# Kernel tuning notes

Hardware: AMD Instinct MI355X
Metric: run time of the kernel (lower is better)

## Reference

```python
import jax, jax.numpy as jnp
import numpy as np

B, N, L, U = 128, 32, 100, 1024  # batch, n agents, traj length, hidden units


def setup_inputs() -> dict:
    key = jax.random.key(0)
    ks = jax.random.split(key, 16)
    s = 0.02
    return {
        "x": jax.random.normal(ks[0], (B, 4 * N, L), dtype=jnp.float32),
        "edges": jax.random.uniform(ks[1], (B, N, N), dtype=jnp.float32),
        # traj MLP: 4*L -> U -> U -> 1  (weights stored as [in, out])
        "traj1_w": s * jax.random.normal(ks[2], (4 * L, U), dtype=jnp.float32),
        "traj1_b": jnp.zeros((U,), dtype=jnp.float32),
        "traj2_w": s * jax.random.normal(ks[3], (U, U), dtype=jnp.float32),
        "traj2_b": jnp.zeros((U,), dtype=jnp.float32),
        "traj3_w": s * jax.random.normal(ks[4], (U, 1), dtype=jnp.float32),
        "traj3_b": jnp.zeros((1,), dtype=jnp.float32),
        # interaction MLP: 8*L -> U -> U -> 1
        "int1_w": s * jax.random.normal(ks[5], (8 * L, U), dtype=jnp.float32),
        "int1_b": jnp.zeros((U,), dtype=jnp.float32),
        "int2_w": s * jax.random.normal(ks[6], (U, U), dtype=jnp.float32),
        "int2_b": jnp.zeros((U,), dtype=jnp.float32),
        "int3_w": s * jax.random.normal(ks[7], (U, 1), dtype=jnp.float32),
        "int3_b": jnp.zeros((1,), dtype=jnp.float32),
    }


def _mlp3(h, w1, b1, w2, b2, w3, b3):
    h = jax.nn.relu(h @ w1 + b1)
    h = jax.nn.relu(h @ w2 + b2)
    return h @ w3 + b3


def reference(x, edges, traj1_w, traj1_b, traj2_w, traj2_b, traj3_w, traj3_b,
              int1_w, int1_b, int2_w, int2_b, int3_w, int3_b):
    b = x.shape[0]
    n = edges.shape[1]
    length = x.shape[2]
    x4 = x.reshape(b, n, 4, length)  # [B, n, 4, L]

    # per-trajectory energy: (B*n, 4*L) -> MLP -> (B, n) -> sum over agents
    te = _mlp3(x4.reshape(b * n, 4 * length),
               traj1_w, traj1_b, traj2_w, traj2_b, traj3_w, traj3_b)
    traj_e = te.reshape(b, n).sum(axis=1, keepdims=True)  # [B, 1]

    # pairwise interaction energy: concat sender/receiver channels -> (B*n*n, 8*L)
    xi = jnp.broadcast_to(x4[:, :, None], (b, n, n, 4, length))  # row index c1
    xj = jnp.broadcast_to(x4[:, None, :], (b, n, n, 4, length))  # col index c2
    pair = jnp.concatenate([xi, xj], axis=3).reshape(b * n * n, 8 * length)
    ie = _mlp3(pair, int1_w, int1_b, int2_w, int2_b, int3_w, int3_b)
    int_e = (edges * ie.reshape(b, n, n)).sum(axis=(1, 2))[:, None]  # [B, 1]

    return traj_e + int_e  # [B, 1]
```

## Files before the change

kernel.cpp:

```cpp
#include <hip/hip_runtime.h>

typedef unsigned short u16;
typedef unsigned int u32;
typedef short bf16x8_t __attribute__((ext_vector_type(8)));
typedef float f32x4_t __attribute__((ext_vector_type(4)));

#define OFF_XB   (0)
#define SZ_XB    (4096*416*2)
#define OFF_WCAT (OFF_XB + SZ_XB)
#define SZ_WCAT  (3072*416*2)
#define OFF_W2T  (OFF_WCAT + SZ_WCAT)
#define SZ_W2    (1024*1024*2)
#define OFF_W2I  (OFF_W2T + SZ_W2)
#define OFF_T1   (OFF_W2I + SZ_W2)
#define SZ_T1    (4096*1024*2)
#define OFF_P    (OFF_T1 + SZ_T1)
#define SZ_PQ    (4096*1024*4)
#define OFF_Q    (OFF_P + SZ_PQ)

__device__ __forceinline__ u16 f2bf(float f) {
  union { float f; u32 u; } v; v.f = f;
  u32 r = v.u + 0x7fffu + ((v.u >> 16) & 1u);
  return (u16)(r >> 16);
}
__device__ __forceinline__ u32 pk2(float a, float b) {
  u32 ua = __float_as_uint(fmaxf(a, 0.f)) + 0x8000u;
  u32 ub = __float_as_uint(fmaxf(b, 0.f)) + 0x8000u;
  return __builtin_amdgcn_perm(ub, ua, 0x07060302);
}
__device__ __forceinline__ void gload_lds16(const void* g, void* l) {
  __builtin_amdgcn_global_load_lds(
      (const __attribute__((address_space(1))) void*)g,
      (__attribute__((address_space(3))) void*)l, 16, 0, 0);
}

__device__ __forceinline__ void stage_sw(const u16* g, int ld, int row0, int k0,
                                         u16* lds, int nrow64, int wave, int lane) {
  int c = ((lane & 3) - ((lane >> 2) & 3)) & 3;
  const u16* src0 = g + (size_t)(row0 + (lane >> 2)) * ld + k0 + c * 8;
#pragma unroll
  for (int it = 0; it < nrow64; ++it) {
    int rbase = it * 64 + wave * 16;
    gload_lds16(src0 + (size_t)rbase * ld, lds + rbase * 32);
  }
}
__device__ __forceinline__ bf16x8_t read_sw(const u16* lds, int row, int quad) {
  int s = (quad + row) & 3;
  return *(const bf16x8_t*)(lds + row * 32 + s * 8);
}

__global__ __launch_bounds__(256) void k_prep(
    const float* __restrict__ x, const float* __restrict__ t1w,
    const float* __restrict__ i1w, const float* __restrict__ t2w,
    const float* __restrict__ i2w, u16* __restrict__ Xb,
    u16* __restrict__ Wcat, u16* __restrict__ W2t, u16* __restrict__ W2i) {
  __shared__ float tb[32][33];
  int gy = blockIdx.y, tid = threadIdx.x;
  if (gy < 4096) {
    int k = blockIdx.x * 256 + tid;
    if (k < 416)
      Xb[(size_t)gy * 416 + k] = (k < 400) ? f2bf(x[(size_t)gy * 400 + k]) : (u16)0;
  } else if (gy < 7168) {
    int n = gy - 4096;
    int k = blockIdx.x * 256 + tid;
    if (k >= 416) return;
    float v = 0.f;
    if (k < 400) {
      if (n < 1024)      v = t1w[(size_t)k * 1024 + n];
      else if (n < 2048) v = i1w[(size_t)k * 1024 + (n - 1024)];
      else               v = i1w[(size_t)(400 + k) * 1024 + (n - 2048)];
    }
    Wcat[(size_t)n * 416 + k] = f2bf(v);
  } else {
    if (blockIdx.x) return;
    int t = gy - 7168;
    const float* W = (t < 1024) ? t2w : i2w;
    u16* Wt = (t < 1024) ? W2t : W2i;
    int tt = t & 1023;
    int n0 = (tt & 31) * 32, k0 = (tt >> 5) * 32;
    int tx = tid & 31, ty = tid >> 5;
#pragma unroll
    for (int i = 0; i < 32; i += 8)
      tb[ty + i][tx] = W[(size_t)(k0 + ty + i) * 1024 + n0 + tx];
    __syncthreads();
#pragma unroll
    for (int i = 0; i < 32; i += 8)
      Wt[(size_t)(n0 + ty + i) * 1024 + k0 + tx] = f2bf(tb[tx][ty + i]);
  }
}

__global__ __launch_bounds__(256) void k_gemm_l1(
    const u16* __restrict__ Xb, const u16* __restrict__ Wt,
    const float* __restrict__ b_t1, const float* __restrict__ b_i1,
    u16* __restrict__ T1, float* __restrict__ Pp, float* __restrict__ Qq) {
  __shared__ __align__(16) u16 al[128 * 32];
  __shared__ __align__(16) u16 bl[128 * 32];
  int tid = threadIdx.x, lane = tid & 63, wave = tid >> 6;
  int wr = wave & 1, wc = wave >> 1, ln = lane & 15, quad = lane >> 4;
  int m0 = blockIdx.x * 128, n0 = blockIdx.y * 128;
  f32x4_t acc[4][4];
#pragma unroll
  for (int i = 0; i < 4; ++i)
#pragma unroll
    for (int j = 0; j < 4; ++j) acc[i][j] = (f32x4_t){0.f, 0.f, 0.f, 0.f};

  for (int k0 = 0; k0 < 416; k0 += 32) {
    stage_sw(Xb, 416, m0, k0, al, 2, wave, lane);
    stage_sw(Wt, 416, n0, k0, bl, 2, wave, lane);
    __syncthreads();
    bf16x8_t af[4], bfr[4];
#pragma unroll
    for (int mt = 0; mt < 4; ++mt)
      af[mt] = read_sw(al, wr * 64 + mt * 16 + ln, quad);
#pragma unroll
    for (int nt = 0; nt < 4; ++nt)
      bfr[nt] = read_sw(bl, wc * 64 + nt * 16 + ln, quad);
#pragma unroll
    for (int mt = 0; mt < 4; ++mt)
#pragma unroll
      for (int nt = 0; nt < 4; ++nt)
        acc[mt][nt] = __builtin_amdgcn_mfma_f32_16x16x32_bf16(af[mt], bfr[nt], acc[mt][nt], 0, 0, 0);
    __syncthreads();
  }
  int seg = n0 >> 10;
#pragma unroll
  for (int nt = 0; nt < 4; ++nt) {
    int n_g = n0 + wc * 64 + nt * 16 + ln;
    int ns = n_g & 1023;
    float bias = (seg == 0) ? b_t1[ns] : (seg == 1 ? b_i1[ns] : 0.f);
#pragma unroll
    for (int mt = 0; mt < 4; ++mt) {
      f32x4_t c = acc[mt][nt];
#pragma unroll
      for (int r = 0; r < 4; ++r) {
        int m_g = m0 + wr * 64 + mt * 16 + quad * 4 + r;
        size_t idx = (size_t)m_g * 1024 + ns;
        float v = c[r] + bias;
        if (seg == 0)      T1[idx] = (u16)((__float_as_uint(fmaxf(v, 0.f)) + 0x8000u) >> 16);
        else if (seg == 1) Pp[idx] = v;
        else               Qq[idx] = v;
      }
    }
  }
}

__global__ __launch_bounds__(256) void k_traj23(
    const u16* __restrict__ T1, const u16* __restrict__ W2t,
    const float* __restrict__ b2, const float* __restrict__ w3,
    const float* __restrict__ b3, float* __restrict__ out) {
  __shared__ __align__(16) u16 al[128 * 32];
  __shared__ __align__(16) u16 bl[128 * 32];
  __shared__ float rowsum[128];
  int tid = threadIdx.x, lane = tid & 63, wave = tid >> 6;
  int wr = wave & 1, wc = wave >> 1, ln = lane & 15, quad = lane >> 4;
  int m0 = blockIdx.x * 128, n0 = blockIdx.y * 128;
  f32x4_t acc[4][4];
#pragma unroll
  for (int i = 0; i < 4; ++i)
#pragma unroll
    for (int j = 0; j < 4; ++j) acc[i][j] = (f32x4_t){0.f, 0.f, 0.f, 0.f};

  for (int k0 = 0; k0 < 1024; k0 += 32) {
    stage_sw(T1, 1024, m0, k0, al, 2, wave, lane);
    stage_sw(W2t, 1024, n0, k0, bl, 2, wave, lane);
    __syncthreads();
    bf16x8_t af[4], bfr[4];
#pragma unroll
    for (int mt = 0; mt < 4; ++mt)
      af[mt] = read_sw(al, wr * 64 + mt * 16 + ln, quad);
#pragma unroll
    for (int nt = 0; nt < 4; ++nt)
      bfr[nt] = read_sw(bl, wc * 64 + nt * 16 + ln, quad);
#pragma unroll
    for (int mt = 0; mt < 4; ++mt)
#pragma unroll
      for (int nt = 0; nt < 4; ++nt)
        acc[mt][nt] = __builtin_amdgcn_mfma_f32_16x16x32_bf16(af[mt], bfr[nt], acc[mt][nt], 0, 0, 0);
    __syncthreads();
  }
  float b2v[4], w3v[4];
#pragma unroll
  for (int nt = 0; nt < 4; ++nt) {
    int n = n0 + wc * 64 + nt * 16 + ln;
    b2v[nt] = b2[n]; w3v[nt] = w3[n];
  }
  if (tid < 128) rowsum[tid] = 0.f;
  __syncthreads();
#pragma unroll
  for (int mt = 0; mt < 4; ++mt) {
    float s[4] = {0.f, 0.f, 0.f, 0.f};
#pragma unroll
    for (int nt = 0; nt < 4; ++nt) {
      f32x4_t c = acc[mt][nt];
#pragma unroll
      for (int r = 0; r < 4; ++r) s[r] += fmaxf(c[r] + b2v[nt], 0.f) * w3v[nt];
    }
#pragma unroll
    for (int r = 0; r < 4; ++r) {
      for (int off = 1; off < 16; off <<= 1) s[r] += __shfl_xor(s[r], off);
      if (ln == 0) atomicAdd(&rowsum[wr * 64 + mt * 16 + quad * 4 + r], s[r]);
    }
  }
  __syncthreads();
  float contrib = 0.f;
  if (tid < 128) contrib = rowsum[tid] + (n0 == 0 ? b3[0] : 0.f);
  for (int off = 1; off < 32; off <<= 1) contrib += __shfl_xor(contrib, off);
  if ((lane & 31) == 0 && tid < 128) atomicAdd(&out[(m0 + tid) >> 5], contrib);
}

#define LDA_H 40
__device__ __forceinline__ void pack_h1(u16* dst, int rloc, int kh,
                                        float4 p0, float4 p1, float4 q0, float4 q1) {
  uint4 w;
  w.x = pk2(p0.x + q0.x, p0.y + q0.y);
  w.y = pk2(p0.z + q0.z, p0.w + q0.w);
  w.z = pk2(p1.x + q1.x, p1.y + q1.y);
  w.w = pk2(p1.z + q1.z, p1.w + q1.w);
  *(uint4*)(dst + rloc * LDA_H + kh) = w;
}

__global__ __launch_bounds__(256) void k_int_fused(
    const float* __restrict__ Pp, const float* __restrict__ Qq,
    const u16* __restrict__ W2t, const float* __restrict__ b2,
    const float* __restrict__ w3, const float* __restrict__ b3,
    const float* __restrict__ edges, float* __restrict__ out) {
  __shared__ __align__(16) u16 h1[2 * 64 * LDA_H];
  __shared__ __align__(16) u16 bl[2 * 256 * 32];
  __shared__ float rowsum[64];
  int tid = threadIdx.x, lane = tid & 63, wave = tid >> 6;
  int ln = lane & 15, quad = lane >> 4;
  int mtile = blockIdx.y;
  int n0 = blockIdx.x * 256;
  int b = mtile >> 4;
  int i0 = (mtile & 15) * 2;

  int rloc = tid >> 2;
  int kh = (tid & 3) * 8;
  const float* prow = Pp + ((size_t)(b * 32 + i0 + (rloc >> 5)) << 10) + kh;
  const float* qrow = Qq + ((size_t)(b * 32 + (rloc & 31)) << 10) + kh;

  f32x4_t acc[4][4];
#pragma unroll
  for (int i = 0; i < 4; ++i)
#pragma unroll
    for (int j = 0; j < 4; ++j) acc[i][j] = (f32x4_t){0.f, 0.f, 0.f, 0.f};

  float4 pA0, pA1, qA0, qA1;
  float4 pB0, pB1, qB0, qB1;

  {
    float4 t0 = *(const float4*)(prow),     t1 = *(const float4*)(prow + 4);
    float4 u0 = *(const float4*)(qrow),     u1 = *(const float4*)(qrow + 4);
    pack_h1(h1, rloc, kh, t0, t1, u0, u1);
    stage_sw(W2t, 1024, n0, 0, bl, 4, wave, lane);
    pA0 = *(const float4*)(prow + 32); pA1 = *(const float4*)(prow + 36);
    qA0 = *(const float4*)(qrow + 32); qA1 = *(const float4*)(qrow + 36);
  }
  __syncthreads();

  for (int kp = 0; kp < 1024; kp += 64) {
    {
      bf16x8_t af[4], bfr[4];
#pragma unroll
      for (int mt = 0; mt < 4; ++mt)
        af[mt] = *(const bf16x8_t*)(h1 + (mt * 16 + ln) * LDA_H + quad * 8);
#pragma unroll
      for (int nt = 0; nt < 4; ++nt)
        bfr[nt] = read_sw(bl, wave * 64 + nt * 16 + ln, quad);
      if (kp + 64 < 1024) {
        pB0 = *(const float4*)(prow + kp + 64); pB1 = *(const float4*)(prow + kp + 68);
        qB0 = *(const float4*)(qrow + kp + 64); qB1 = *(const float4*)(qrow + kp + 68);
      }
      stage_sw(W2t, 1024, n0, kp + 32, bl + 256 * 32, 4, wave, lane);
#pragma unroll
      for (int mt = 0; mt < 4; ++mt)
#pragma unroll
        for (int nt = 0; nt < 4; ++nt)
          acc[mt][nt] = __builtin_amdgcn_mfma_f32_16x16x32_bf16(af[mt], bfr[nt], acc[mt][nt], 0, 0, 0);
      pack_h1(h1 + 64 * LDA_H, rloc, kh, pA0, pA1, qA0, qA1);
      __syncthreads();
    }
    {
      bf16x8_t af[4], bfr[4];
#pragma unroll
      for (int mt = 0; mt < 4; ++mt)
        af[mt] = *(const bf16x8_t*)(h1 + 64 * LDA_H + (mt * 16 + ln) * LDA_H + quad * 8);
#pragma unroll
      for (int nt = 0; nt < 4; ++nt)
        bfr[nt] = read_sw(bl + 256 * 32, wave * 64 + nt * 16 + ln, quad);
      if (kp + 96 < 1024) {
        pA0 = *(const float4*)(prow + kp + 96); pA1 = *(const float4*)(prow + kp + 100);
        qA0 = *(const float4*)(qrow + kp + 96); qA1 = *(const float4*)(qrow + kp + 100);
      }
      if (kp + 64 < 1024)
        stage_sw(W2t, 1024, n0, kp + 64, bl, 4, wave, lane);
#pragma unroll
      for (int mt = 0; mt < 4; ++mt)
#pragma unroll
        for (int nt = 0; nt < 4; ++nt)
          acc[mt][nt] = __builtin_amdgcn_mfma_f32_16x16x32_bf16(af[mt], bfr[nt], acc[mt][nt], 0, 0, 0);
      if (kp + 64 < 1024)
        pack_h1(h1, rloc, kh, pB0, pB1, qB0, qB1);
      __syncthreads();
    }
  }

  float b2v[4], w3v[4];
#pragma unroll
  for (int nt = 0; nt < 4; ++nt) {
    int n = n0 + wave * 64 + nt * 16 + ln;
    b2v[nt] = b2[n]; w3v[nt] = w3[n];
  }
  if (tid < 64) rowsum[tid] = 0.f;
  __syncthreads();
#pragma unroll
  for (int mt = 0; mt < 4; ++mt) {
    float s[4] = {0.f, 0.f, 0.f, 0.f};
#pragma unroll
    for (int nt = 0; nt < 4; ++nt) {
      f32x4_t c = acc[mt][nt];
#pragma unroll
      for (int r = 0; r < 4; ++r) s[r] += fmaxf(c[r] + b2v[nt], 0.f) * w3v[nt];
    }
#pragma unroll
    for (int r = 0; r < 4; ++r) {
      for (int off = 1; off < 16; off <<= 1) s[r] += __shfl_xor(s[r], off);
      if (ln == 0) atomicAdd(&rowsum[mt * 16 + quad * 4 + r], s[r]);
    }
  }
  __syncthreads();
  if (wave == 0) {
    float ie = rowsum[lane] + (n0 == 0 ? b3[0] : 0.f);
    int i = i0 + (lane >> 5), j = lane & 31;
    float contrib = edges[(size_t)b * 1024 + i * 32 + j] * ie;
    for (int off = 1; off < 64; off <<= 1) contrib += __shfl_xor(contrib, off);
    if (lane == 0) atomicAdd(&out[b], contrib);
  }
}

extern "C" void kernel_launch(void* const* d_in, const int* in_sizes, int n_in,
                              void* d_out, int out_size, void* d_ws, size_t ws_size,
                              hipStream_t stream) {
  const float* x   = (const float*)d_in[0];
  const float* edges = (const float*)d_in[1];
  const float* t1w = (const float*)d_in[2];
  const float* t1b = (const float*)d_in[3];
  const float* t2w = (const float*)d_in[4];
  const float* t2b = (const float*)d_in[5];
  const float* t3w = (const float*)d_in[6];
  const float* t3b = (const float*)d_in[7];
  const float* i1w = (const float*)d_in[8];
  const float* i1b = (const float*)d_in[9];
  const float* i2w = (const float*)d_in[10];
  const float* i2b = (const float*)d_in[11];
  const float* i3w = (const float*)d_in[12];
  const float* i3b = (const float*)d_in[13];
  char* ws = (char*)d_ws;
  u16*   Xb   = (u16*)(ws + OFF_XB);
  u16*   Wcat = (u16*)(ws + OFF_WCAT);
  u16*   W2t  = (u16*)(ws + OFF_W2T);
  u16*   W2i  = (u16*)(ws + OFF_W2I);
  u16*   T1   = (u16*)(ws + OFF_T1);
  float* Pp   = (float*)(ws + OFF_P);
  float* Qq   = (float*)(ws + OFF_Q);
  float* out  = (float*)d_out;

  hipMemsetAsync(out, 0, 128 * sizeof(float), stream);
  k_prep<<<dim3(2, 9216), 256, 0, stream>>>(x, t1w, i1w, t2w, i2w, Xb, Wcat, W2t, W2i);
  k_gemm_l1<<<dim3(32, 24), 256, 0, stream>>>(Xb, Wcat, t1b, i1b, T1, Pp, Qq);
  k_traj23<<<dim3(32, 8), 256, 0, stream>>>(T1, W2t, t2b, t3w, t3b, out);
  k_int_fused<<<dim3(4, 2048), 256, 0, stream>>>(Pp, Qq, W2i, i2b, i3w, i3b, edges, out);
}
```

Baseline: 583.3 us.

## Load interaction W2 fragments directly from global in k-blocked layout, drop LDS staging

```diff
diff --git a/kernel.cpp b/kernel.cpp
--- a/kernel.cpp
+++ b/kernel.cpp
@@ -53,7 +53,7 @@
     const float* __restrict__ x, const float* __restrict__ t1w,
     const float* __restrict__ i1w, const float* __restrict__ t2w,
     const float* __restrict__ i2w, u16* __restrict__ Xb,
-    u16* __restrict__ Wcat, u16* __restrict__ W2t, u16* __restrict__ W2i) {
+    u16* __restrict__ Wcat, u16* __restrict__ W2t, u16* __restrict__ W2k) {
   __shared__ float tb[32][33];
   int gy = blockIdx.y, tid = threadIdx.x;
   if (gy < 4096) {
@@ -74,18 +74,23 @@
   } else {
     if (blockIdx.x) return;
     int t = gy - 7168;
-    const float* W = (t < 1024) ? t2w : i2w;
-    u16* Wt = (t < 1024) ? W2t : W2i;
     int tt = t & 1023;
     int n0 = (tt & 31) * 32, k0 = (tt >> 5) * 32;
     int tx = tid & 31, ty = tid >> 5;
+    const float* W = (t < 1024) ? t2w : i2w;
 #pragma unroll
     for (int i = 0; i < 32; i += 8)
       tb[ty + i][tx] = W[(size_t)(k0 + ty + i) * 1024 + n0 + tx];
     __syncthreads();
-#pragma unroll
-    for (int i = 0; i < 32; i += 8)
-      Wt[(size_t)(n0 + ty + i) * 1024 + k0 + tx] = f2bf(tb[tx][ty + i]);
+    if (t < 1024) {
+#pragma unroll
+      for (int i = 0; i < 32; i += 8)
+        W2t[(size_t)(n0 + ty + i) * 1024 + k0 + tx] = f2bf(tb[tx][ty + i]);
+    } else {
+#pragma unroll
+      for (int i = 0; i < 32; i += 8)
+        W2k[(size_t)(k0 >> 5) * 32768 + (size_t)(n0 + ty + i) * 32 + tx] = f2bf(tb[tx][ty + i]);
+    }
   }
 }
 
@@ -221,11 +226,10 @@
 
 __global__ __launch_bounds__(256) void k_int_fused(
     const float* __restrict__ Pp, const float* __restrict__ Qq,
-    const u16* __restrict__ W2t, const float* __restrict__ b2,
+    const u16* __restrict__ W2k, const float* __restrict__ b2,
     const float* __restrict__ w3, const float* __restrict__ b3,
     const float* __restrict__ edges, float* __restrict__ out) {
   __shared__ __align__(16) u16 h1[2 * 64 * LDA_H];
-  __shared__ __align__(16) u16 bl[2 * 256 * 32];
   __shared__ float rowsum[64];
   int tid = threadIdx.x, lane = tid & 63, wave = tid >> 6;
   int ln = lane & 15, quad = lane >> 4;
@@ -238,6 +242,7 @@
   int kh = (tid & 3) * 8;
   const float* prow = Pp + ((size_t)(b * 32 + i0 + (rloc >> 5)) << 10) + kh;
   const float* qrow = Qq + ((size_t)(b * 32 + (rloc & 31)) << 10) + kh;
+  const u16* bptr = W2k + (size_t)(n0 + wave * 64 + ln) * 32 + quad * 8;
 
   f32x4_t acc[4][4];
 #pragma unroll
@@ -245,62 +250,64 @@
 #pragma unroll
     for (int j = 0; j < 4; ++j) acc[i][j] = (f32x4_t){0.f, 0.f, 0.f, 0.f};
 
-  float4 pA0, pA1, qA0, qA1;
-  float4 pB0, pB1, qB0, qB1;
-
+  bf16x8_t bA[4], bB[4];
   {
     float4 t0 = *(const float4*)(prow),     t1 = *(const float4*)(prow + 4);
     float4 u0 = *(const float4*)(qrow),     u1 = *(const float4*)(qrow + 4);
     pack_h1(h1, rloc, kh, t0, t1, u0, u1);
-    stage_sw(W2t, 1024, n0, 0, bl, 4, wave, lane);
-    pA0 = *(const float4*)(prow + 32); pA1 = *(const float4*)(prow + 36);
-    qA0 = *(const float4*)(qrow + 32); qA1 = *(const float4*)(qrow + 36);
-  }
-  __syncthreads();
-
+#pragma unroll
+    for (int nt = 0; nt < 4; ++nt)
+      bA[nt] = *(const bf16x8_t*)(bptr + nt * 512);
+  }
+  __syncthreads();
+
+  float4 pN0, pN1, qN0, qN1;
   for (int kp = 0; kp < 1024; kp += 64) {
     {
-      bf16x8_t af[4], bfr[4];
+      int k0 = kp;
+      bf16x8_t af[4];
 #pragma unroll
       for (int mt = 0; mt < 4; ++mt)
         af[mt] = *(const bf16x8_t*)(h1 + (mt * 16 + ln) * LDA_H + quad * 8);
-#pragma unroll
-      for (int nt = 0; nt < 4; ++nt)
-        bfr[nt] = read_sw(bl, wave * 64 + nt * 16 + ln, quad);
-      if (kp + 64 < 1024) {
-        pB0 = *(const float4*)(prow + kp + 64); pB1 = *(const float4*)(prow + kp + 68);
-        qB0 = *(const float4*)(qrow + kp + 64); qB1 = *(const float4*)(qrow + kp + 68);
+      if (k0 + 32 < 1024) {
+        pN0 = *(const float4*)(prow + k0 + 32); pN1 = *(const float4*)(prow + k0 + 36);
+        qN0 = *(const float4*)(qrow + k0 + 32); qN1 = *(const float4*)(qrow + k0 + 36);
+        const u16* bp = bptr + (size_t)((k0 >> 5) + 1) * 32768;
+#pragma unroll
+        for (int nt = 0; nt < 4; ++nt)
+          bB[nt] = *(const bf16x8_t*)(bp + nt * 512);
       }
-      stage_sw(W2t, 1024, n0, kp + 32, bl + 256 * 32, 4, wave, lane);
 #pragma unroll
       for (int mt = 0; mt < 4; ++mt)
 #pragma unroll
         for (int nt = 0; nt < 4; ++nt)
-          acc[mt][nt] = __builtin_amdgcn_mfma_f32_16x16x32_bf16(af[mt], bfr[nt], acc[mt][nt], 0, 0, 0);
-      pack_h1(h1 + 64 * LDA_H, rloc, kh, pA0, pA1, qA0, qA1);
+          acc[mt][nt] = __builtin_amdgcn_mfma_f32_16x16x32_bf16(af[mt], bA[nt], acc[mt][nt], 0, 0, 0);
+      if (k0 + 32 < 1024)
+        pack_h1(h1 + 64 * LDA_H, rloc, kh, pN0, pN1, qN0, qN1);
       __syncthreads();
     }
     {
-      bf16x8_t af[4], bfr[4];
+      int k0 = kp + 32;
+      if (k0 >= 1024) break;
+      bf16x8_t af[4];
 #pragma unroll
       for (int mt = 0; mt < 4; ++mt)
         af[mt] = *(const bf16x8_t*)(h1 + 64 * LDA_H + (mt * 16 + ln) * LDA_H + quad * 8);
-#pragma unroll
-      for (int nt = 0; nt < 4; ++nt)
-        bfr[nt] = read_sw(bl + 256 * 32, wave * 64 + nt * 16 + ln, quad);
-      if (kp + 96 < 1024) {
-        pA0 = *(const float4*)(prow + kp + 96); pA1 = *(const float4*)(prow + kp + 100);
-        qA0 = *(const float4*)(qrow + kp + 96); qA1 = *(const float4*)(qrow + kp + 100);
+      if (k0 + 32 < 1024) {
+        pN0 = *(const float4*)(prow + k0 + 32); pN1 = *(const float4*)(prow + k0 + 36);
+        qN0 = *(const float4*)(qrow + k0 + 32); qN1 = *(const float4*)(qrow + k0 + 36);
+        const u16* bp = bptr + (size_t)((k0 >> 5) + 1) * 32768;
+#pragma unroll
+        for (int nt = 0; nt < 4; ++nt)
+          bA[nt] = *(const bf16x8_t*)(bp + nt * 512);
       }
-      if (kp + 64 < 1024)
-        stage_sw(W2t, 1024, n0, kp + 64, bl, 4, wave, lane);
 #pragma unroll
       for (int mt = 0; mt < 4; ++mt)
 #pragma unroll
         for (int nt = 0; nt < 4; ++nt)
-          acc[mt][nt] = __builtin_amdgcn_mfma_f32_16x16x32_bf16(af[mt], bfr[nt], acc[mt][nt], 0, 0, 0);
-      if (kp + 64 < 1024)
-        pack_h1(h1, rloc, kh, pB0, pB1, qB0, qB1);
+          acc[mt][nt] = __builtin_amdgcn_mfma_f32_16x16x32_bf16(af[mt], bB[nt], acc[mt][nt], 0, 0, 0);
+      if (k0 + 32 < 1024)
+        pack_h1(h1, rloc, kh, pN0, pN1, qN0, qN1);
       __syncthreads();
     }
   }
@@ -359,15 +366,15 @@
   u16*   Xb   = (u16*)(ws + OFF_XB);
   u16*   Wcat = (u16*)(ws + OFF_WCAT);
   u16*   W2t  = (u16*)(ws + OFF_W2T);
-  u16*   W2i  = (u16*)(ws + OFF_W2I);
+  u16*   W2k  = (u16*)(ws + OFF_W2I);
   u16*   T1   = (u16*)(ws + OFF_T1);
   float* Pp   = (float*)(ws + OFF_P);
   float* Qq   = (float*)(ws + OFF_Q);
   float* out  = (float*)d_out;
 
   hipMemsetAsync(out, 0, 128 * sizeof(float), stream);
-  k_prep<<<dim3(2, 9216), 256, 0, stream>>>(x, t1w, i1w, t2w, i2w, Xb, Wcat, W2t, W2i);
+  k_prep<<<dim3(2, 9216), 256, 0, stream>>>(x, t1w, i1w, t2w, i2w, Xb, Wcat, W2t, W2k);
   k_gemm_l1<<<dim3(32, 24), 256, 0, stream>>>(Xb, Wcat, t1b, i1b, T1, Pp, Qq);
   k_traj23<<<dim3(32, 8), 256, 0, stream>>>(T1, W2t, t2b, t3w, t3b, out);
-  k_int_fused<<<dim3(4, 2048), 256, 0, stream>>>(Pp, Qq, W2i, i2b, i3w, i3b, edges, out);
-}
+  k_int_fused<<<dim3(4, 2048), 256, 0, stream>>>(Pp, Qq, W2k, i2b, i3w, i3b, edges, out);
+}
```

Result: slower. 602.1 us (+3.2%).
